# Kernel optimization log

Measured on AMD Instinct MI355X. Metric: run time of the kernel, lower is better.

## Reference

```python
import jax, jax.numpy as jnp
import numpy as np

B, C, D, H, W = 8, 1, 128, 160, 128

def setup_inputs() -> dict:
    key = jax.random.key(0)
    kx, kb = jax.random.split(key)
    x = jax.random.normal(kx, (B, C, D, H, W), dtype=jnp.float32)
    base_volume = jax.random.normal(kb, (C, D, H, W), dtype=jnp.float32)
    return {"x": x, "base_volume": base_volume}

def reference(x, base_volume):
    # skimage match_histograms for continuous float images reduces (for a.e.-unique
    # values) to: map each source voxel's empirical CDF quantile onto the template's
    # inverse CDF via linear interpolation.
    tmpl = base_volume.ravel()
    t_sorted = jnp.sort(tmpl)                      # template inverse-CDF values
    M = tmpl.shape[0]
    tq = jnp.arange(1, M + 1, dtype=x.dtype) / M   # template CDF quantiles

    def match_one(sample):
        flat = sample.ravel()
        N = flat.shape[0]
        # rank of each voxel within its own sample (double argsort)
        ranks = jnp.argsort(jnp.argsort(flat))
        q = (ranks + 1).astype(flat.dtype) / N     # source empirical CDF
        matched = jnp.interp(q, tq, t_sorted)
        return matched.reshape(sample.shape)

    matched_vol = jax.vmap(match_one)(x)
    # self.model is identity here (the kernel headroom is the matching itself)
    return matched_vol
```

## Files before the change

### kernel.cpp

```cpp
#include <hip/hip_runtime.h>
#include <stdint.h>


#define SEG_N 2621440
#define NSEG 9
#define TILE 4096
#define NBLK (SEG_N / TILE)
#define RADIX 256
#define HL (RADIX * NBLK)
#define SCHUNK 4096
#define SNB (HL / SCHUNK)
#define SBUF (TILE + (TILE >> 4))

__device__ __forceinline__ uint32_t fkey(float f) {
  uint32_t b = __float_as_uint(f);
  return b ^ ((b & 0x80000000u) ? 0xFFFFFFFFu : 0x80000000u);
}
__device__ __forceinline__ float finv(uint32_t u) {
  uint32_t b = u ^ ((u & 0x80000000u) ? 0x80000000u : 0xFFFFFFFFu);
  return __uint_as_float(b);
}
__device__ __forceinline__ uint32_t SIDX(uint32_t i) { return i + (i >> 4); }

__global__ __launch_bounds__(256) void init_k(const float* __restrict__ x,
                                              const float* __restrict__ tmpl,
                                              int segbase,
                                              uint64_t* __restrict__ pairsA,
                                              uint32_t* __restrict__ Hkb) {
  __shared__ uint32_t hw[4 * RADIX];
  const int t = threadIdx.x;
  const int blk = blockIdx.x;
  const int sl = blockIdx.y;
  const int seg = segbase + sl;
  const float* src = (seg == 0) ? tmpl : (x + (size_t)(seg - 1) * SEG_N);
  uint64_t* pa = pairsA + (size_t)sl * SEG_N;
  hw[t] = 0; hw[t + 256] = 0; hw[t + 512] = 0; hw[t + 768] = 0;
  __syncthreads();
  const int w = t >> 6;
  const uint32_t base = blk * TILE;
  const float4* s4 = reinterpret_cast<const float4*>(src + base);
#pragma unroll
  for (int r = 0; r < 4; ++r) {
    float4 v = s4[r * 256 + t];
    uint32_t i0 = base + (uint32_t)(r * 256 + t) * 4u;
    float f[4] = {v.x, v.y, v.z, v.w};
#pragma unroll
    for (int c = 0; c < 4; ++c) {
      uint32_t k = fkey(f[c]);
      atomicAdd(&hw[w * 256 + (k & 255u)], 1u);
      pa[i0 + c] = ((uint64_t)k << 32) | (uint64_t)(i0 + c);
    }
  }
  __syncthreads();
  Hkb[(size_t)sl * HL + (size_t)blk * RADIX + t] =
      hw[t] + hw[t + 256] + hw[t + 512] + hw[t + 768];
}

__global__ __launch_bounds__(256) void hist_k(const uint64_t* __restrict__ pairs,
                                              uint32_t* __restrict__ Hkb, int p) {
  __shared__ uint32_t hw[4 * RADIX];
  const int t = threadIdx.x;
  const int blk = blockIdx.x;
  const int sl = blockIdx.y;
  hw[t] = 0; hw[t + 256] = 0; hw[t + 512] = 0; hw[t + 768] = 0;
  __syncthreads();
  const int w = t >> 6;
  const int sh = 32 + 8 * p;
  const ulonglong2* pc = reinterpret_cast<const ulonglong2*>(
      pairs + (size_t)sl * SEG_N + (size_t)blk * TILE);
#pragma unroll
  for (int r = 0; r < 8; ++r) {
    ulonglong2 v = pc[r * 256 + t];
    atomicAdd(&hw[w * 256 + ((uint32_t)(v.x >> sh) & 255u)], 1u);
    atomicAdd(&hw[w * 256 + ((uint32_t)(v.y >> sh) & 255u)], 1u);
  }
  __syncthreads();
  Hkb[(size_t)sl * HL + (size_t)blk * RADIX + t] =
      hw[t] + hw[t + 256] + hw[t + 512] + hw[t + 768];
}

__global__ __launch_bounds__(256) void scanT_k(const uint32_t* __restrict__ Hkb,
                                               uint32_t* __restrict__ Hbk,
                                               uint32_t* __restrict__ desc) {
  __shared__ uint32_t lds[256];
  __shared__ uint32_t baseS;
  const int t = threadIdx.x;
  const int c = blockIdx.x;
  const int sl = blockIdx.y;
  const uint32_t* src = Hkb + (size_t)sl * HL;
  const uint32_t e0 = (uint32_t)c * SCHUNK + (uint32_t)t * 16;
  uint32_t vals[16];
  uint32_t s = 0;
#pragma unroll
  for (int i = 0; i < 16; ++i) {
    uint32_t e = e0 + (uint32_t)i;
    uint32_t bin = e / NBLK, blk = e - bin * NBLK;
    vals[i] = src[(size_t)blk * RADIX + bin];
    s += vals[i];
  }
  lds[t] = s;
  __syncthreads();
#pragma unroll
  for (int off = 1; off < 256; off <<= 1) {
    uint32_t a = (t >= off) ? lds[t - off] : 0u;
    __syncthreads();
    lds[t] += a;
    __syncthreads();
  }
  const uint32_t incl = lds[t];
  const uint32_t total = lds[255];
  const uint32_t ex = incl - s;

  uint32_t* dseg = desc + sl * SNB;
  if (t == 0) {
    __hip_atomic_store(&dseg[c], (total & 0x3FFFFFFFu) |
                                     ((c == 0 ? 2u : 1u) << 30),
                       __ATOMIC_RELAXED, __HIP_MEMORY_SCOPE_AGENT);
    uint32_t acc = 0;
    if (c > 0) {
      int b = c - 1;
      for (;;) {
        uint32_t v;
        do {
          v = __hip_atomic_load(&dseg[b], __ATOMIC_RELAXED,
                                __HIP_MEMORY_SCOPE_AGENT);
        } while ((v >> 30) == 0u);
        acc += v & 0x3FFFFFFFu;
        if ((v >> 30) == 2u) break;
        --b;
      }
      __hip_atomic_store(&dseg[c], ((acc + total) & 0x3FFFFFFFu) | (2u << 30),
                         __ATOMIC_RELAXED, __HIP_MEMORY_SCOPE_AGENT);
    }
    baseS = acc;
  }
  __syncthreads();
  uint32_t run = baseS + ex;
  uint32_t* dst = Hbk + (size_t)sl * HL + e0;
#pragma unroll
  for (int i = 0; i < 16; ++i) {
    dst[i] = run;
    run += vals[i];
  }
}

template <int P, int MODE>
__global__ __launch_bounds__(256) void part_k(const uint64_t* __restrict__ src,
                                              uint64_t* __restrict__ dst,
                                              const uint32_t* __restrict__ Hbk,
                                              float* __restrict__ tsorted,
                                              float* __restrict__ out,
                                              int segbase, int slbase) {
  __shared__ uint64_t buf[SBUF];
  __shared__ uint32_t ldsStart[RADIX];
  __shared__ uint32_t ldsBase[RADIX];
  __shared__ uint32_t scanS[48];
  const int t = threadIdx.x;
  const int blk = blockIdx.x;
  const int sl = slbase + blockIdx.y;
  const int seg = segbase + sl;
  const uint64_t* ps = src + (size_t)sl * SEG_N + (size_t)blk * TILE;

  ldsBase[t] = Hbk[(size_t)sl * HL + (size_t)t * NBLK + blk];

#pragma unroll
  for (int r = 0; r < 16; ++r) buf[SIDX(r * 256 + t)] = ps[r * 256 + t];
  __syncthreads();

  uint64_t e[16];
  const int lane = t & 63, w = t >> 6;
#pragma unroll
  for (int rnd = 0; rnd < 2; ++rnd) {
    const int sh = 32 + 8 * P + 4 * rnd;
#pragma unroll
    for (int j = 0; j < 16; ++j) e[j] = buf[SIDX(t * 16 + j)];
    uint32_t cntW[4] = {0u, 0u, 0u, 0u};
#pragma unroll
    for (int j = 0; j < 16; ++j) {
      uint32_t d4 = (uint32_t)(e[j] >> sh) & 15u;
      cntW[d4 >> 2] += 1u << ((d4 & 3u) * 8u);
    }
    uint32_t v[8], a[8];
#pragma unroll
    for (int q = 0; q < 8; ++q) {
      uint32_t word = cntW[q >> 1];
      uint32_t s2 = (q & 1) * 16;
      v[q] = ((word >> s2) & 0xffu) | (((word >> (s2 + 8)) & 0xffu) << 16);
      a[q] = v[q];
    }
#pragma unroll
    for (int o = 1; o < 64; o <<= 1) {
#pragma unroll
      for (int q = 0; q < 8; ++q) {
        uint32_t n = __shfl_up(a[q], (unsigned)o, 64);
        if (lane >= o) a[q] += n;
      }
    }
    if (lane == 63) {
#pragma unroll
      for (int q = 0; q < 8; ++q) scanS[w * 8 + q] = a[q];
    }
    __syncthreads();
    if (t == 0) {
      uint32_t run = 0;
#pragma unroll
      for (int q = 0; q < 8; ++q) {
        uint32_t r0 = 0;
#pragma unroll
        for (int ww = 0; ww < 4; ++ww) {
          uint32_t xv = scanS[ww * 8 + q];
          scanS[ww * 8 + q] = r0;
          r0 += xv;
        }
        uint32_t b0 = r0 & 0xffffu, b1 = r0 >> 16;
        scanS[32 + q] = run | ((run + b0) << 16);
        run += b0 + b1;
      }
    }
    __syncthreads();
    uint64_t posW[4];
#pragma unroll
    for (int q = 0; q < 8; ++q) {
      uint32_t exq = a[q] - v[q] + scanS[w * 8 + q];
      uint32_t base = scanS[32 + q];
      uint32_t p0 = (base & 0xffffu) + (exq & 0xffffu);
      uint32_t p1 = (base >> 16) + (exq >> 16);
      uint64_t pk = (uint64_t)p0 | ((uint64_t)p1 << 16);
      if ((q & 1) == 0) posW[q >> 1] = pk;
      else posW[q >> 1] |= pk << 32;
    }
#pragma unroll
    for (int j = 0; j < 16; ++j) {
      uint32_t d4 = (uint32_t)(e[j] >> sh) & 15u;
      uint32_t hi = d4 >> 2;
      uint32_t fs = (d4 & 3u) * 16u;
      uint32_t p = (uint32_t)(posW[hi] >> fs) & 0xffffu;
      posW[hi] += (uint64_t)1 << fs;
      buf[SIDX(p)] = e[j];
    }
    __syncthreads();
  }

  const uint8_t* b8 = reinterpret_cast<const uint8_t*>(buf);
#pragma unroll
  for (int r = 0; r < 16; ++r) {
    uint32_t s = (uint32_t)(r * 256 + t);
    e[r] = buf[SIDX(s)];
    uint32_t d = (uint32_t)(e[r] >> (32 + 8 * P)) & 255u;
    uint32_t dp = (s == 0) ? 0x100u
                           : (uint32_t)b8[(size_t)SIDX(s - 1) * 8 + 4 + P];
    if (d != dp) ldsStart[d] = s;
  }
  __syncthreads();

#pragma unroll
  for (int r = 0; r < 16; ++r) {
    uint32_t s = (uint32_t)(r * 256 + t);
    uint64_t el = e[r];
    uint32_t key = (uint32_t)(el >> 32);
    uint32_t d = (key >> (8 * P)) & 255u;
    uint32_t dest = ldsBase[d] + s - ldsStart[d];
    if (MODE == 0) {
      dst[(size_t)sl * SEG_N + dest] = el;
    } else if (MODE == 1) {
      tsorted[dest] = finv(key);
    } else {
      out[(size_t)(seg - 1) * SEG_N + (uint32_t)el] = tsorted[dest];
    }
  }
}

extern "C" void kernel_launch(void* const* d_in, const int* in_sizes, int n_in,
                              void* d_out, int out_size, void* d_ws, size_t ws_size,
                              hipStream_t stream) {
  const float* x = (const float*)d_in[0];
  const float* tmpl = (const float*)d_in[1];
  float* out = (float*)d_out;

  auto need = [](int nb) -> size_t {
    return (size_t)nb * ((size_t)SEG_N * 16 + (size_t)HL * 8 + 4096) +
           (size_t)SEG_N * 4 + 16384;
  };
  const int nb = (ws_size >= need(9)) ? 9 : (ws_size >= need(3)) ? 3 : 1;

  uint8_t* w = (uint8_t*)d_ws;
  size_t off = 0;
  auto carve = [&](size_t bytes) -> void* {
    void* p = w + off;
    off = (off + bytes + 255) & ~(size_t)255;
    return p;
  };
  uint64_t* pairsA = (uint64_t*)carve((size_t)nb * SEG_N * 8);
  uint64_t* pairsB = (uint64_t*)carve((size_t)nb * SEG_N * 8);
  uint32_t* Hkb = (uint32_t*)carve((size_t)nb * HL * 4);
  uint32_t* Hbk = (uint32_t*)carve((size_t)nb * HL * 4);
  uint32_t* desc = (uint32_t*)carve((size_t)4 * nb * SNB * 4);
  float* tsorted = (float*)carve((size_t)SEG_N * 4);

  for (int g = 0; g < NSEG; g += nb) {
    const dim3 gi(NBLK, nb);
    const dim3 gs(SNB, nb);

    hipMemsetAsync(desc, 0, (size_t)4 * nb * SNB * 4, stream);

    init_k<<<gi, 256, 0, stream>>>(x, tmpl, g, pairsA, Hkb);
    scanT_k<<<gs, 256, 0, stream>>>(Hkb, Hbk, desc + 0 * nb * SNB);
    part_k<0, 0><<<gi, 256, 0, stream>>>(pairsA, pairsB, Hbk, tsorted, out, g, 0);
    hist_k<<<gi, 256, 0, stream>>>(pairsB, Hkb, 1);
    scanT_k<<<gs, 256, 0, stream>>>(Hkb, Hbk, desc + 1 * nb * SNB);
    part_k<1, 0><<<gi, 256, 0, stream>>>(pairsB, pairsA, Hbk, tsorted, out, g, 0);
    hist_k<<<gi, 256, 0, stream>>>(pairsA, Hkb, 2);
    scanT_k<<<gs, 256, 0, stream>>>(Hkb, Hbk, desc + 2 * nb * SNB);
    part_k<2, 0><<<gi, 256, 0, stream>>>(pairsA, pairsB, Hbk, tsorted, out, g, 0);
    hist_k<<<gi, 256, 0, stream>>>(pairsB, Hkb, 3);
    scanT_k<<<gs, 256, 0, stream>>>(Hkb, Hbk, desc + 3 * nb * SNB);
    if (g == 0) {
      part_k<3, 1><<<dim3(NBLK, 1), 256, 0, stream>>>(pairsB, pairsA, Hbk,
                                                      tsorted, out, g, 0);
      if (nb > 1)
        part_k<3, 2><<<dim3(NBLK, nb - 1), 256, 0, stream>>>(pairsB, pairsA, Hbk,
                                                             tsorted, out, g, 1);
    } else {
      part_k<3, 2><<<dim3(NBLK, nb), 256, 0, stream>>>(pairsB, pairsA, Hbk,
                                                       tsorted, out, g, 0);
    }
  }
}
```

Baseline: 1.162 ms.

## Rework local radix split, batch lookback loads, add wave-aggregated histogram for top digit

Changes the in-block local sort from two 4-bit rounds with packed 16-counter scans to four 2-bit rounds, each using a small two-value packed wave scan. This cuts shuffle work and register pressure per round but doubles the number of LDS scatter passes and barriers. The decoupled lookback in the scan kernel now issues up to eight descriptor loads at once instead of polling them one at a time, to reduce serial latency. The top-digit histogram pass uses ballot-based wave aggregation to cut LDS atomic contention on the highly skewed most-significant byte, at the cost of a loop per wave.

```diff
diff --git a/kernel.cpp b/kernel.cpp
--- a/kernel.cpp
+++ b/kernel.cpp
@@ -56,8 +56,21 @@
       hw[t] + hw[t + 256] + hw[t + 512] + hw[t + 768];
 }
 
+__device__ __forceinline__ void wf_count(uint32_t d, uint32_t* hist) {
+  const int lane = threadIdx.x & 63;
+  uint64_t rem = ~0ull;
+  while (rem) {
+    uint32_t lead = (uint32_t)__ffsll((unsigned long long)rem) - 1u;
+    uint32_t d0 = (uint32_t)__shfl((int)d, (int)lead, 64);
+    uint64_t eq = __ballot(d == d0);
+    if (lane == (int)lead) atomicAdd(&hist[d0], (uint32_t)__popcll(eq));
+    rem &= ~eq;
+  }
+}
+
+template <int P>
 __global__ __launch_bounds__(256) void hist_k(const uint64_t* __restrict__ pairs,
-                                              uint32_t* __restrict__ Hkb, int p) {
+                                              uint32_t* __restrict__ Hkb) {
   __shared__ uint32_t hw[4 * RADIX];
   const int t = threadIdx.x;
   const int blk = blockIdx.x;
@@ -65,14 +78,21 @@
   hw[t] = 0; hw[t + 256] = 0; hw[t + 512] = 0; hw[t + 768] = 0;
   __syncthreads();
   const int w = t >> 6;
-  const int sh = 32 + 8 * p;
+  const int sh = 32 + 8 * P;
   const ulonglong2* pc = reinterpret_cast<const ulonglong2*>(
       pairs + (size_t)sl * SEG_N + (size_t)blk * TILE);
 #pragma unroll
   for (int r = 0; r < 8; ++r) {
     ulonglong2 v = pc[r * 256 + t];
-    atomicAdd(&hw[w * 256 + ((uint32_t)(v.x >> sh) & 255u)], 1u);
-    atomicAdd(&hw[w * 256 + ((uint32_t)(v.y >> sh) & 255u)], 1u);
+    uint32_t d0 = (uint32_t)(v.x >> sh) & 255u;
+    uint32_t d1 = (uint32_t)(v.y >> sh) & 255u;
+    if (P == 3) {
+      wf_count(d0, &hw[w * 256]);
+      wf_count(d1, &hw[w * 256]);
+    } else {
+      atomicAdd(&hw[w * 256 + d0], 1u);
+      atomicAdd(&hw[w * 256 + d1], 1u);
+    }
   }
   __syncthreads();
   Hkb[(size_t)sl * HL + (size_t)blk * RADIX + t] =
@@ -119,15 +139,25 @@
     uint32_t acc = 0;
     if (c > 0) {
       int b = c - 1;
-      for (;;) {
-        uint32_t v;
-        do {
-          v = __hip_atomic_load(&dseg[b], __ATOMIC_RELAXED,
-                                __HIP_MEMORY_SCOPE_AGENT);
-        } while ((v >> 30) == 0u);
-        acc += v & 0x3FFFFFFFu;
-        if ((v >> 30) == 2u) break;
-        --b;
+      bool done = false;
+      while (!done) {
+        uint32_t dv[8];
+        const int n = (b >= 7) ? 8 : (b + 1);
+#pragma unroll
+        for (int i = 0; i < 8; ++i)
+          if (i < n)
+            dv[i] = __hip_atomic_load(&dseg[b - i], __ATOMIC_RELAXED,
+                                      __HIP_MEMORY_SCOPE_AGENT);
+        for (int i = 0; i < n; ++i) {
+          uint32_t v = dv[i];
+          while ((v >> 30) == 0u)
+            v = __hip_atomic_load(&dseg[b - i], __ATOMIC_RELAXED,
+                                  __HIP_MEMORY_SCOPE_AGENT);
+          acc += v & 0x3FFFFFFFu;
+          if ((v >> 30) == 2u) { done = true; break; }
+        }
+        b -= n;
+        if (!done && b < 0) break;
       }
       __hip_atomic_store(&dseg[c], ((acc + total) & 0x3FFFFFFFu) | (2u << 30),
                          __ATOMIC_RELAXED, __HIP_MEMORY_SCOPE_AGENT);
@@ -142,6 +172,36 @@
     dst[i] = run;
     run += vals[i];
   }
+}
+
+__device__ __forceinline__ void scan_pack2(uint32_t v0, uint32_t v1, uint32_t* s,
+                                           uint32_t& ex0, uint32_t& ex1,
+                                           uint32_t& tot0, uint32_t& tot1) {
+  const int lane = threadIdx.x & 63, w = threadIdx.x >> 6;
+  uint32_t a = v0, b = v1;
+#pragma unroll
+  for (int o = 1; o < 64; o <<= 1) {
+    uint32_t na = __shfl_up(a, (unsigned)o, 64);
+    uint32_t nb = __shfl_up(b, (unsigned)o, 64);
+    if (lane >= o) { a += na; b += nb; }
+  }
+  if (lane == 63) { s[w] = a; s[4 + w] = b; }
+  __syncthreads();
+  if (threadIdx.x == 0) {
+    uint32_t r0 = 0, r1 = 0;
+#pragma unroll
+    for (int i = 0; i < 4; ++i) {
+      uint32_t q0 = s[i], q1 = s[4 + i];
+      s[i] = r0; s[4 + i] = r1;
+      r0 += q0; r1 += q1;
+    }
+    s[8] = r0; s[9] = r1;
+  }
+  __syncthreads();
+  ex0 = a - v0 + s[w];
+  ex1 = b - v1 + s[4 + w];
+  tot0 = s[8]; tot1 = s[9];
+  __syncthreads();
 }
 
 template <int P, int MODE>
@@ -154,7 +214,7 @@
   __shared__ uint64_t buf[SBUF];
   __shared__ uint32_t ldsStart[RADIX];
   __shared__ uint32_t ldsBase[RADIX];
-  __shared__ uint32_t scanS[48];
+  __shared__ uint32_t scanS[12];
   const int t = threadIdx.x;
   const int blk = blockIdx.x;
   const int sl = slbase + blockIdx.y;
@@ -168,75 +228,30 @@
   __syncthreads();
 
   uint64_t e[16];
-  const int lane = t & 63, w = t >> 6;
-#pragma unroll
-  for (int rnd = 0; rnd < 2; ++rnd) {
-    const int sh = 32 + 8 * P + 4 * rnd;
+#pragma unroll
+  for (int rnd = 0; rnd < 4; ++rnd) {
 #pragma unroll
     for (int j = 0; j < 16; ++j) e[j] = buf[SIDX(t * 16 + j)];
-    uint32_t cntW[4] = {0u, 0u, 0u, 0u};
+    uint32_t cnt[4] = {0u, 0u, 0u, 0u};
 #pragma unroll
     for (int j = 0; j < 16; ++j) {
-      uint32_t d4 = (uint32_t)(e[j] >> sh) & 15u;
-      cntW[d4 >> 2] += 1u << ((d4 & 3u) * 8u);
-    }
-    uint32_t v[8], a[8];
-#pragma unroll
-    for (int q = 0; q < 8; ++q) {
-      uint32_t word = cntW[q >> 1];
-      uint32_t s2 = (q & 1) * 16;
-      v[q] = ((word >> s2) & 0xffu) | (((word >> (s2 + 8)) & 0xffu) << 16);
-      a[q] = v[q];
-    }
-#pragma unroll
-    for (int o = 1; o < 64; o <<= 1) {
-#pragma unroll
-      for (int q = 0; q < 8; ++q) {
-        uint32_t n = __shfl_up(a[q], (unsigned)o, 64);
-        if (lane >= o) a[q] += n;
-      }
-    }
-    if (lane == 63) {
-#pragma unroll
-      for (int q = 0; q < 8; ++q) scanS[w * 8 + q] = a[q];
-    }
-    __syncthreads();
-    if (t == 0) {
-      uint32_t run = 0;
-#pragma unroll
-      for (int q = 0; q < 8; ++q) {
-        uint32_t r0 = 0;
-#pragma unroll
-        for (int ww = 0; ww < 4; ++ww) {
-          uint32_t xv = scanS[ww * 8 + q];
-          scanS[ww * 8 + q] = r0;
-          r0 += xv;
-        }
-        uint32_t b0 = r0 & 0xffffu, b1 = r0 >> 16;
-        scanS[32 + q] = run | ((run + b0) << 16);
-        run += b0 + b1;
-      }
-    }
-    __syncthreads();
-    uint64_t posW[4];
-#pragma unroll
-    for (int q = 0; q < 8; ++q) {
-      uint32_t exq = a[q] - v[q] + scanS[w * 8 + q];
-      uint32_t base = scanS[32 + q];
-      uint32_t p0 = (base & 0xffffu) + (exq & 0xffffu);
-      uint32_t p1 = (base >> 16) + (exq >> 16);
-      uint64_t pk = (uint64_t)p0 | ((uint64_t)p1 << 16);
-      if ((q & 1) == 0) posW[q >> 1] = pk;
-      else posW[q >> 1] |= pk << 32;
-    }
+      uint32_t d2 = (uint32_t)(e[j] >> (32 + 8 * P + 2 * rnd)) & 3u;
+      cnt[d2]++;
+    }
+    uint32_t p0 = cnt[0] | (cnt[1] << 16);
+    uint32_t p1 = cnt[2] | (cnt[3] << 16);
+    uint32_t ex0, ex1, tot0, tot1;
+    scan_pack2(p0, p1, scanS, ex0, ex1, tot0, tot1);
+    uint32_t t0 = tot0 & 0xffffu, t1 = tot0 >> 16, t2 = tot1 & 0xffffu;
+    uint32_t pos[4];
+    pos[0] = (ex0 & 0xffffu);
+    pos[1] = t0 + (ex0 >> 16);
+    pos[2] = t0 + t1 + (ex1 & 0xffffu);
+    pos[3] = t0 + t1 + t2 + (ex1 >> 16);
 #pragma unroll
     for (int j = 0; j < 16; ++j) {
-      uint32_t d4 = (uint32_t)(e[j] >> sh) & 15u;
-      uint32_t hi = d4 >> 2;
-      uint32_t fs = (d4 & 3u) * 16u;
-      uint32_t p = (uint32_t)(posW[hi] >> fs) & 0xffffu;
-      posW[hi] += (uint64_t)1 << fs;
-      buf[SIDX(p)] = e[j];
+      uint32_t d2 = (uint32_t)(e[j] >> (32 + 8 * P + 2 * rnd)) & 3u;
+      buf[SIDX(pos[d2]++)] = e[j];
     }
     __syncthreads();
   }
@@ -306,13 +321,13 @@
     init_k<<<gi, 256, 0, stream>>>(x, tmpl, g, pairsA, Hkb);
     scanT_k<<<gs, 256, 0, stream>>>(Hkb, Hbk, desc + 0 * nb * SNB);
     part_k<0, 0><<<gi, 256, 0, stream>>>(pairsA, pairsB, Hbk, tsorted, out, g, 0);
-    hist_k<<<gi, 256, 0, stream>>>(pairsB, Hkb, 1);
+    hist_k<1><<<gi, 256, 0, stream>>>(pairsB, Hkb);
     scanT_k<<<gs, 256, 0, stream>>>(Hkb, Hbk, desc + 1 * nb * SNB);
     part_k<1, 0><<<gi, 256, 0, stream>>>(pairsB, pairsA, Hbk, tsorted, out, g, 0);
-    hist_k<<<gi, 256, 0, stream>>>(pairsA, Hkb, 2);
+    hist_k<2><<<gi, 256, 0, stream>>>(pairsA, Hkb);
     scanT_k<<<gs, 256, 0, stream>>>(Hkb, Hbk, desc + 2 * nb * SNB);
     part_k<2, 0><<<gi, 256, 0, stream>>>(pairsA, pairsB, Hbk, tsorted, out, g, 0);
-    hist_k<<<gi, 256, 0, stream>>>(pairsB, Hkb, 3);
+    hist_k<3><<<gi, 256, 0, stream>>>(pairsB, Hkb);
     scanT_k<<<gs, 256, 0, stream>>>(Hkb, Hbk, desc + 3 * nb * SNB);
     if (g == 0) {
       part_k<3, 1><<<dim3(NBLK, 1), 256, 0, stream>>>(pairsB, pairsA, Hbk,
```

Result: no change. 1.185 ms (+1.9%).
